# Optimization experiments

Measured on AMD Instinct MI355X. Metric: run time of the kernel, lower is better.

The kernel has to match this reference:

```python
import math
import jax, jax.numpy as jnp
import numpy as np

H = 1024
N = 64
DT_MIN, DT_MAX = 0.001, 0.1
L_CONST = 4096


def setup_inputs() -> dict:
    key = jax.random.key(0)
    k1, k2 = jax.random.split(key)
    log_dt = jax.random.uniform(k1, (H,), dtype=jnp.float32) * (
        math.log(DT_MAX) - math.log(DT_MIN)
    ) + math.log(DT_MIN)
    C = jax.random.normal(k2, (H, N // 2, 2), dtype=jnp.float32)  # real view of complex C
    log_A_real = jnp.log(0.5 * jnp.ones((H, N // 2), dtype=jnp.float32))
    A_imag = math.pi * jnp.tile(jnp.arange(N // 2, dtype=jnp.float32)[None, :], (H, 1))
    return {"L": L_CONST, "log_dt": log_dt, "C": C, "log_A_real": log_A_real, "A_imag": A_imag}


def reference(L, log_dt, C, log_A_real, A_imag):
    dt = jnp.exp(log_dt)                                  # (H,)
    Cc = C[..., 0] + 1j * C[..., 1]                        # (H, N/2) complex
    A = -jnp.exp(log_A_real) + 1j * A_imag                 # (H, N/2) complex
    dtA = A * dt[:, None]                                  # (H, N/2)
    t = jnp.arange(L, dtype=jnp.float32)                   # (L,)
    exp_dtA_t = jnp.exp(dtA[:, :, None] * t)               # (H, N/2, L) complex Vandermonde
    C_eff = Cc * (jnp.exp(dtA) - 1.0) / A                  # (H, N/2)
    K = 2.0 * jnp.einsum('hn,hnl->hl', C_eff, exp_dtA_t).real  # (H, L)
    return K
```

## Files before the change

kernel.cpp:

```cpp
#include <hip/hip_runtime.h>
#include <math.h>

#define NH 32

typedef _Float16 f16;
typedef _Float16 f16x2 __attribute__((ext_vector_type(2)));
typedef _Float16 f16x4 __attribute__((ext_vector_type(4)));
typedef float    f32x4 __attribute__((ext_vector_type(4)));

__device__ __forceinline__ float reduce2pi(float x) {
    const float INV2PI = 0.15915494309189535f;
    const float PI2_HI = 6.28125f;
    const float PI2_LO = 1.9353071795864769e-3f;
    float k = rintf(x * INV2PI);
    float r = fmaf(-k, PI2_HI, x);
    r = fmaf(-k, PI2_LO, r);
    return r;
}

__global__ __launch_bounds__(256, 4) void s4d_kernel(
    const float* __restrict__ log_dt,
    const float* __restrict__ Cv,
    const float* __restrict__ log_A_real,
    const float* __restrict__ A_imag,
    float* __restrict__ Kout,
    int L)
{
    const int h   = blockIdx.x;
    const int tid = threadIdx.x;

    __shared__ f16 Alds[32][68];
    __shared__ f16 Wlds[128][68];
    __shared__ float s_dar[NH], s_dai[NH];
    __shared__ float s_zr[NH],  s_zi[NH];
    __shared__ float s_ur[NH],  s_ui[NH];
    __shared__ float s_cer[NH], s_cei[NH];
    __shared__ float s_e1r[NH], s_e1i[NH];
    __shared__ float s_e2r[NH], s_e2i[NH];

    if (tid < 128) {
        const int n = tid & 31;
        const int j = tid >> 5;
        const float dt  = __expf(log_dt[h]);
        const float Ar  = -__expf(log_A_real[h * NH + n]);
        const float Ai  = A_imag[h * NH + n];
        const float dar = Ar * dt;
        const float dai = Ai * dt;
        const float S = (j == 0) ? 1.0f : (j == 1) ? 128.0f
                      : (j == 2) ? 1024.0f : 2048.0f;
        float e = __expf(dar * S);
        float sn, cs;
        __sincosf(reduce2pi(dai * S), &sn, &cs);
        float vr = e * cs, vi = e * sn;
        if (j == 0) {
            s_dar[n] = dar;  s_dai[n] = dai;
            s_zr[n] = vr;    s_zi[n] = vi;
            float edr = vr - 1.0f, edi = vi;
            float inv = 1.0f / fmaf(Ar, Ar, Ai * Ai);
            float fr  = (edr * Ar + edi * Ai) * inv;
            float fi  = (edi * Ar - edr * Ai) * inv;
            float cr  = Cv[(h * NH + n) * 2 + 0];
            float ci  = Cv[(h * NH + n) * 2 + 1];
            s_cer[n] = 2.0f * (cr * fr - ci * fi);
            s_cei[n] = 2.0f * (cr * fi + ci * fr);
        } else if (j == 1) { s_ur[n]  = vr;  s_ui[n]  = vi; }
        else if   (j == 2) { s_e1r[n] = vr;  s_e1i[n] = vi; }
        else               { s_e2r[n] = vr;  s_e2i[n] = vi; }
    }
    __syncthreads();

    const int lane = tid & 63;
    const int wv   = tid >> 6;

    if (lane < NH) {
        const int n = lane;
        float sr, si;
        if      (wv == 0) { sr = 1.0f;      si = 0.0f; }
        else if (wv == 1) { sr = s_e1r[n];  si = s_e1i[n]; }
        else if (wv == 2) { sr = s_e2r[n];  si = s_e2i[n]; }
        else {
            sr = s_e2r[n] * s_e1r[n] - s_e2i[n] * s_e1i[n];
            si = s_e2r[n] * s_e1i[n] + s_e2i[n] * s_e1r[n];
        }
        float gr = s_cer[n] * sr - s_cei[n] * si;
        float gi = s_cer[n] * si + s_cei[n] * sr;
        const float ur = s_ur[n], ui = s_ui[n];
        #pragma unroll
        for (int s = 0; s < 8; ++s) {
            const int a = wv * 8 + s;
            f16x2 pg = { (f16)gr, (f16)(-gi) };
            *reinterpret_cast<f16x2*>(&Alds[a][2 * n]) = pg;
            float t = gr * ur - gi * ui;
            gi = gr * ui + gi * ur;
            gr = t;
        }
    }

    {
        const int n  = tid & 31;
        const int bg = tid >> 5;
        const float b0f = (float)(bg * 16);
        float e0 = __expf(s_dar[n] * b0f);
        float sn, cs;
        __sincosf(s_dai[n] * b0f, &sn, &cs);
        float wr = e0 * cs, wi = e0 * sn;
        const float zr = s_zr[n], zi = s_zi[n];
        #pragma unroll
        for (int i = 0; i < 16; ++i) {
            const int b = bg * 16 + i;
            f16x2 pw = { (f16)wr, (f16)wi };
            *reinterpret_cast<f16x2*>(&Wlds[b][2 * n]) = pw;
            float t = wr * zr - wi * zi;
            wi = wr * zi + wi * zr;
            wr = t;
        }
    }
    __syncthreads();

    const int r = lane & 15;
    const int q = lane >> 4;
    float* outp = Kout + (size_t)h * (size_t)L;
    #pragma unroll
    for (int mi = 0; mi < 2; ++mi) {
        #pragma unroll
        for (int ni = 0; ni < 2; ++ni) {
            f32x4 acc = {0.f, 0.f, 0.f, 0.f};
            #pragma unroll
            for (int ks = 0; ks < 4; ++ks) {
                f16x4 xf = *(const f16x4*)&Wlds[32 * wv + 16 * mi + r][16 * ks + 4 * q];
                f16x4 yf = *(const f16x4*)&Alds[16 * ni + r][16 * ks + 4 * q];
                acc = __builtin_amdgcn_mfma_f32_16x16x16f16(xf, yf, acc, 0, 0, 0);
            }
            const int a  = 16 * ni + r;
            const int b0 = 32 * wv + 16 * mi + 4 * q;
            *(f32x4*)&outp[(size_t)a * 128 + b0] = acc;
        }
    }
}

extern "C" void kernel_launch(void* const* d_in, const int* in_sizes, int n_in,
                              void* d_out, int out_size, void* d_ws, size_t ws_size,
                              hipStream_t stream) {
    const float* log_dt     = (const float*)d_in[1];
    const float* Cv         = (const float*)d_in[2];
    const float* log_A_real = (const float*)d_in[3];
    const float* A_imag     = (const float*)d_in[4];
    float* Kout = (float*)d_out;

    const int Hn = in_sizes[1];
    const int L  = out_size / Hn;

    dim3 grid(Hn), block(256);
    hipLaunchKernelGGL(s4d_kernel, grid, block, 0, stream,
                       log_dt, Cv, log_A_real, A_imag, Kout, L);
}
```

Before: 11.33 us.

## Drop first barrier by recomputing params per thread, stage output via LDS

The shared-memory parameter precompute and its barrier are removed. Each thread now recomputes dt, A, z, C_eff and its starting powers in registers, trading redundant transcendental work for one fewer synchronisation. MFMA results are staged in an LDS tile and written out as fully contiguous 512-byte rows with nontemporal stores instead of scattered 16-byte stores. This adds an extra barrier and about 17 KB of LDS, which may lower occupancy.

```diff
diff --git a/kernel.cpp b/kernel.cpp
--- a/kernel.cpp
+++ b/kernel.cpp
@@ -26,65 +26,74 @@
     float* __restrict__ Kout,
     int L)
 {
-    const int h   = blockIdx.x;
-    const int tid = threadIdx.x;
+    const int h    = blockIdx.x;
+    const int tid  = threadIdx.x;
+    const int lane = tid & 63;
+    const int wv   = tid >> 6;
 
     __shared__ f16 Alds[32][68];
     __shared__ f16 Wlds[128][68];
-    __shared__ float s_dar[NH], s_dai[NH];
-    __shared__ float s_zr[NH],  s_zi[NH];
-    __shared__ float s_ur[NH],  s_ui[NH];
-    __shared__ float s_cer[NH], s_cei[NH];
-    __shared__ float s_e1r[NH], s_e1i[NH];
-    __shared__ float s_e2r[NH], s_e2i[NH];
+    __shared__ float s_out[32][132];
 
-    if (tid < 128) {
-        const int n = tid & 31;
-        const int j = tid >> 5;
+    {
+        const int n  = tid & 31;
+        const int bg = tid >> 5;
         const float dt  = __expf(log_dt[h]);
         const float Ar  = -__expf(log_A_real[h * NH + n]);
         const float Ai  = A_imag[h * NH + n];
         const float dar = Ar * dt;
         const float dai = Ai * dt;
-        const float S = (j == 0) ? 1.0f : (j == 1) ? 128.0f
-                      : (j == 2) ? 1024.0f : 2048.0f;
-        float e = __expf(dar * S);
-        float sn, cs;
-        __sincosf(reduce2pi(dai * S), &sn, &cs);
-        float vr = e * cs, vi = e * sn;
-        if (j == 0) {
-            s_dar[n] = dar;  s_dai[n] = dai;
-            s_zr[n] = vr;    s_zi[n] = vi;
-            float edr = vr - 1.0f, edi = vi;
-            float inv = 1.0f / fmaf(Ar, Ar, Ai * Ai);
-            float fr  = (edr * Ar + edi * Ai) * inv;
-            float fi  = (edi * Ar - edr * Ai) * inv;
-            float cr  = Cv[(h * NH + n) * 2 + 0];
-            float ci  = Cv[(h * NH + n) * 2 + 1];
-            s_cer[n] = 2.0f * (cr * fr - ci * fi);
-            s_cei[n] = 2.0f * (cr * fi + ci * fr);
-        } else if (j == 1) { s_ur[n]  = vr;  s_ui[n]  = vi; }
-        else if   (j == 2) { s_e1r[n] = vr;  s_e1i[n] = vi; }
-        else               { s_e2r[n] = vr;  s_e2i[n] = vi; }
+        float zr, zi;
+        {
+            float e = __expf(dar);
+            float sn, cs; __sincosf(dai, &sn, &cs);
+            zr = e * cs;  zi = e * sn;
+        }
+        const float b0f = (float)(bg * 16);
+        float e0 = __expf(dar * b0f);
+        float sn, cs; __sincosf(reduce2pi(dai * b0f), &sn, &cs);
+        float wr = e0 * cs, wi = e0 * sn;
+        #pragma unroll
+        for (int i = 0; i < 16; ++i) {
+            const int b = bg * 16 + i;
+            f16x2 pw = { (f16)wr, (f16)wi };
+            *reinterpret_cast<f16x2*>(&Wlds[b][2 * n]) = pw;
+            float t = wr * zr - wi * zi;
+            wi = wr * zi + wi * zr;
+            wr = t;
+        }
     }
-    __syncthreads();
-
-    const int lane = tid & 63;
-    const int wv   = tid >> 6;
 
     if (lane < NH) {
         const int n = lane;
-        float sr, si;
-        if      (wv == 0) { sr = 1.0f;      si = 0.0f; }
-        else if (wv == 1) { sr = s_e1r[n];  si = s_e1i[n]; }
-        else if (wv == 2) { sr = s_e2r[n];  si = s_e2i[n]; }
-        else {
-            sr = s_e2r[n] * s_e1r[n] - s_e2i[n] * s_e1i[n];
-            si = s_e2r[n] * s_e1i[n] + s_e2i[n] * s_e1r[n];
+        const float dt  = __expf(log_dt[h]);
+        const float Ar  = -__expf(log_A_real[h * NH + n]);
+        const float Ai  = A_imag[h * NH + n];
+        const float dar = Ar * dt;
+        const float dai = Ai * dt;
+        float zr, zi;
+        {
+            float e = __expf(dar);
+            float sn, cs; __sincosf(dai, &sn, &cs);
+            zr = e * cs;  zi = e * sn;
         }
-        float gr = s_cer[n] * sr - s_cei[n] * si;
-        float gi = s_cer[n] * si + s_cei[n] * sr;
-        const float ur = s_ur[n], ui = s_ui[n];
+        float edr = zr - 1.0f, edi = zi;
+        float inv = 1.0f / fmaf(Ar, Ar, Ai * Ai);
+        float fr  = (edr * Ar + edi * Ai) * inv;
+        float fi  = (edi * Ar - edr * Ai) * inv;
+        float cr  = Cv[(h * NH + n) * 2 + 0];
+        float ci  = Cv[(h * NH + n) * 2 + 1];
+        float cer = 2.0f * (cr * fr - ci * fi);
+        float cei = 2.0f * (cr * fi + ci * fr);
+        float eu = __expf(dar * 128.0f);
+        float su, cu; __sincosf(reduce2pi(dai * 128.0f), &su, &cu);
+        float ur = eu * cu, ui = eu * su;
+        const float S = (float)(1024 * wv);
+        float es = __expf(dar * S);
+        float ss, sc; __sincosf(reduce2pi(dai * S), &ss, &sc);
+        float br = es * sc, bi = es * ss;
+        float gr = cer * br - cei * bi;
+        float gi = cer * bi + cei * br;
         #pragma unroll
         for (int s = 0; s < 8; ++s) {
             const int a = wv * 8 + s;
@@ -95,31 +104,10 @@
             gr = t;
         }
     }
-
-    {
-        const int n  = tid & 31;
-        const int bg = tid >> 5;
-        const float b0f = (float)(bg * 16);
-        float e0 = __expf(s_dar[n] * b0f);
-        float sn, cs;
-        __sincosf(s_dai[n] * b0f, &sn, &cs);
-        float wr = e0 * cs, wi = e0 * sn;
-        const float zr = s_zr[n], zi = s_zi[n];
-        #pragma unroll
-        for (int i = 0; i < 16; ++i) {
-            const int b = bg * 16 + i;
-            f16x2 pw = { (f16)wr, (f16)wi };
-            *reinterpret_cast<f16x2*>(&Wlds[b][2 * n]) = pw;
-            float t = wr * zr - wi * zi;
-            wi = wr * zi + wi * zr;
-            wr = t;
-        }
-    }
     __syncthreads();
 
     const int r = lane & 15;
     const int q = lane >> 4;
-    float* outp = Kout + (size_t)h * (size_t)L;
     #pragma unroll
     for (int mi = 0; mi < 2; ++mi) {
         #pragma unroll
@@ -133,8 +121,18 @@
             }
             const int a  = 16 * ni + r;
             const int b0 = 32 * wv + 16 * mi + 4 * q;
-            *(f32x4*)&outp[(size_t)a * 128 + b0] = acc;
+            *(f32x4*)&s_out[a][b0] = acc;
         }
+    }
+    __syncthreads();
+
+    float* outp = Kout + (size_t)h * (size_t)L;
+    #pragma unroll
+    for (int s = 0; s < 4; ++s) {
+        const int a = wv * 8 + 2 * s + (lane >> 5);
+        const int c = (lane & 31) * 4;
+        f32x4 v = *(const f32x4*)&s_out[a][c];
+        __builtin_nontemporal_store(v, (f32x4*)&outp[(size_t)a * 128 + c]);
     }
 }
 
```

Result: faster. 10.26 us, median of 2 (-9.5%).
